# Performance work log

Measured on AMD Instinct MI355X. Metric: run time of the kernel, lower is better.

Reference implementation:

```python
import jax, jax.numpy as jnp
import numpy as np

C_M, C_Z, H, W_LOCAL, G = 256, 128, 8, 32, 16
D = C_M // H  # 32
NEG = -1e9


def setup_inputs() -> dict:
    key = jax.random.key(0)
    ks = jax.random.split(key, 12)
    B, S, N = 1, 32, 512
    s = 0.02
    return {
        "msa": jax.random.normal(ks[0], (B, S, N, C_M), jnp.float32),
        "pair": jax.random.normal(ks[1], (B, N, N, C_Z), jnp.float32),
        "w_q": jax.random.normal(ks[2], (C_M, C_M), jnp.float32) * s,
        "b_q": jnp.zeros((C_M,), jnp.float32),
        "w_k": jax.random.normal(ks[3], (C_M, C_M), jnp.float32) * s,
        "b_k": jnp.zeros((C_M,), jnp.float32),
        "w_v": jax.random.normal(ks[4], (C_M, C_M), jnp.float32) * s,
        "b_v": jnp.zeros((C_M,), jnp.float32),
        "w_o": jax.random.normal(ks[5], (C_M, C_M), jnp.float32) * s,
        "b_o": jnp.zeros((C_M,), jnp.float32),
        "w_b": jax.random.normal(ks[6], (C_Z, H), jnp.float32) * s,
        "b_b": jnp.zeros((H,), jnp.float32),
        "ln_g": jnp.ones((C_M,), jnp.float32),
        "ln_b": jnp.zeros((C_M,), jnp.float32),
    }


def reference(msa, pair, w_q, b_q, w_k, b_k, w_v, b_v, w_o, b_o, w_b, b_b, ln_g, ln_b):
    B, S, N, _ = msa.shape
    # pair bias: [B, N, N, c_z] -> [B, H, N, N]
    bias = jnp.einsum("bnmc,ch->bhnm", pair, w_b) + b_b[None, :, None, None]
    # structured sparsity: local window + global tokens
    i = jnp.arange(N)
    allowed = (jnp.abs(i[:, None] - i[None, :]) <= W_LOCAL // 2) | (i[:, None] < G) | (i[None, :] < G)
    # projections, vectorized over all MSA rows (replaces the per-row python loop)
    q = (msa @ w_q + b_q).reshape(B, S, N, H, D)
    k = (msa @ w_k + b_k).reshape(B, S, N, H, D)
    v = (msa @ w_v + b_v).reshape(B, S, N, H, D)
    scores = jnp.einsum("bsnhd,bsmhd->bshnm", q, k) / jnp.sqrt(jnp.float32(D))
    scores = scores + bias[:, None]  # broadcast over MSA rows
    scores = jnp.where(allowed, scores, NEG)
    attn = jax.nn.softmax(scores, axis=-1)
    out = jnp.einsum("bshnm,bsmhd->bsnhd", attn, v).reshape(B, S, N, C_M)
    out = out @ w_o + b_o
    # residual + LayerNorm over c_m
    y = msa + out
    mu = jnp.mean(y, axis=-1, keepdims=True)
    var = jnp.mean(jnp.square(y - mu), axis=-1, keepdims=True)
    return (y - mu) * jax.lax.rsqrt(var + 1e-5) * ln_g + ln_b
```

## Files before the change

### kernel.cpp

```cpp
#include <hip/hip_runtime.h>
#include <hip/hip_bf16.h>
#include <math.h>

#define NH      8
#define HD      32
#define NN      512
#define SS      32
#define CM      256
#define CZ      128
#define NG      16
#define W_HALF  16
#define MROWS   (SS * NN)

typedef __attribute__((ext_vector_type(8))) __bf16 bf16x8;
typedef __attribute__((ext_vector_type(4))) float f32x4;

__device__ inline unsigned short f2bf(float x) {
    __hip_bfloat16 h = __float2bfloat16(x);
    return __builtin_bit_cast(unsigned short, h);
}
__device__ inline float bflo(unsigned u) { return __uint_as_float(u << 16); }
__device__ inline float bfhi(unsigned u) { return __uint_as_float(u & 0xffff0000u); }
__device__ inline float bf1(unsigned short u) { return __uint_as_float((unsigned)u << 16); }

__global__ __launch_bounds__(256) void cvt_msa_kernel(
    const float* __restrict__ in, unsigned short* __restrict__ out)
{
    int i = (blockIdx.x * 256 + threadIdx.x) * 8;
    const float4* p = reinterpret_cast<const float4*>(in + i);
    float4 v0 = p[0], v1 = p[1];
    union { unsigned short u[8]; uint4 q; } o;
    o.u[0] = f2bf(v0.x); o.u[1] = f2bf(v0.y); o.u[2] = f2bf(v0.z); o.u[3] = f2bf(v0.w);
    o.u[4] = f2bf(v1.x); o.u[5] = f2bf(v1.y); o.u[6] = f2bf(v1.z); o.u[7] = f2bf(v1.w);
    *reinterpret_cast<uint4*>(out + i) = o.q;
}

__global__ __launch_bounds__(256) void cvt_wT_kernel(
    const float* __restrict__ w0, const float* __restrict__ w1,
    const float* __restrict__ w2, const float* __restrict__ w3,
    unsigned short* __restrict__ o0, unsigned short* __restrict__ o1,
    unsigned short* __restrict__ o2, unsigned short* __restrict__ o3)
{
    int mat = blockIdx.y;
    const float* in = (mat == 0) ? w0 : (mat == 1) ? w1 : (mat == 2) ? w2 : w3;
    unsigned short* out = (mat == 0) ? o0 : (mat == 1) ? o1 : (mat == 2) ? o2 : o3;
    int o = blockIdx.x * 256 + threadIdx.x;
    int n = o >> 8, k = o & 255;
    out[o] = f2bf(in[k * 256 + n]);
}

#define JOBS_D  (512 * 33)
#define JOBS_G  (512 * 16)
#define JOBS_R  (512 * 16)
#define NJOBS   (JOBS_D + JOBS_G + JOBS_R)

__global__ __launch_bounds__(256) void bias_kernel(
    const float* __restrict__ pair,
    const float* __restrict__ w_b,
    const float* __restrict__ b_b,
    float* __restrict__ biasD,
    float* __restrict__ biasG,
    float* __restrict__ biasR)
{
    const int t = threadIdx.x;
    const int wave = t >> 6, lane = t & 63;
    int job = blockIdx.x * 4 + wave;
    if (job >= NJOBS) return;

    int n, m;
    float* oaddr;
    int hstride;
    if (job < JOBS_D) {
        n = job / 33;
        int o = job - n * 33;
        m = n + o - 16;
        if (m < 0 || m >= 512) return;
        oaddr = biasD + o * 512 + n;
        hstride = 33 * 512;
    } else if (job < JOBS_D + JOBS_G) {
        int i = job - JOBS_D;
        n = i >> 4; m = i & 15;
        oaddr = biasG + m * 512 + n;
        hstride = 16 * 512;
    } else {
        int i = job - (JOBS_D + JOBS_G);
        n = i & 15; m = i >> 4;
        oaddr = biasR + n * 512 + m;
        hstride = 16 * 512;
    }

    const float2 pv = *reinterpret_cast<const float2*>(
        pair + ((size_t)n * 512 + m) * CZ + 2 * lane);
    const float4 a0 = ((const float4*)(w_b + (2 * lane) * NH))[0];
    const float4 a1 = ((const float4*)(w_b + (2 * lane) * NH))[1];
    const float4 b0 = ((const float4*)(w_b + (2 * lane + 1) * NH))[0];
    const float4 b1 = ((const float4*)(w_b + (2 * lane + 1) * NH))[1];

    float acc8[8];
    acc8[0] = pv.x * a0.x + pv.y * b0.x;
    acc8[1] = pv.x * a0.y + pv.y * b0.y;
    acc8[2] = pv.x * a0.z + pv.y * b0.z;
    acc8[3] = pv.x * a0.w + pv.y * b0.w;
    acc8[4] = pv.x * a1.x + pv.y * b1.x;
    acc8[5] = pv.x * a1.y + pv.y * b1.y;
    acc8[6] = pv.x * a1.z + pv.y * b1.z;
    acc8[7] = pv.x * a1.w + pv.y * b1.w;
#pragma unroll
    for (int h = 0; h < 8; ++h) {
#pragma unroll
        for (int off = 1; off < 64; off <<= 1)
            acc8[h] += __shfl_xor(acc8[h], off, 64);
    }
    if (lane < 8) {
        float v = acc8[0];
#pragma unroll
        for (int h = 1; h < 8; ++h) v = (lane == h) ? acc8[h] : v;
        oaddr[(size_t)lane * hstride] = v + b_b[lane];
    }
}

template <bool RESID, bool BF16OUT>
__global__ __launch_bounds__(256) void mfma_gemm_kernel(
    const unsigned short* __restrict__ A,
    const unsigned short* __restrict__ WT,
    const float* __restrict__ bias,
    const float* __restrict__ resid,
    void* __restrict__ Cout)
{
    __shared__ __align__(16) unsigned short lds[12288];

    const int t = threadIdx.x;
    const int l = t & 63;
    const int w = t >> 6;
    const int wm = w >> 1, wn = w & 1;
    const int bn0 = blockIdx.x * 64;
    const int bm0 = blockIdx.y * 128;

    f32x4 acc[4][2] = {};

    for (int k0 = 0; k0 < 256; k0 += 64) {
#pragma unroll
        for (int j = 0; j < 4; ++j) {
            int Lbase = (j * 4 + w) * 1024;
            int L = Lbase + l * 16;
            int row = L >> 7;
            int cs = (L >> 4) & 7;
            int c = cs ^ (row & 7);
            const unsigned short* gp = A + (size_t)(bm0 + row) * 256 + k0 + c * 8;
            __builtin_amdgcn_global_load_lds(
                (const __attribute__((address_space(1))) void*)gp,
                (__attribute__((address_space(3))) void*)((char*)lds + Lbase), 16, 0, 0);
        }
#pragma unroll
        for (int j = 0; j < 2; ++j) {
            int Lbase = 16384 + (j * 4 + w) * 1024;
            int L = (Lbase - 16384) + l * 16;
            int row = L >> 7;
            int cs = (L >> 4) & 7;
            int c = cs ^ (row & 7);
            const unsigned short* gp = WT + (size_t)(bn0 + row) * 256 + k0 + c * 8;
            __builtin_amdgcn_global_load_lds(
                (const __attribute__((address_space(1))) void*)gp,
                (__attribute__((address_space(3))) void*)((char*)lds + Lbase), 16, 0, 0);
        }
        __syncthreads();

#pragma unroll
        for (int kh = 0; kh < 2; ++kh) {
            bf16x8 a[4], b[2];
#pragma unroll
            for (int m = 0; m < 4; ++m) {
                int row = wm * 64 + m * 16 + (l & 15);
                int c = (kh * 4 + (l >> 4)) ^ (row & 7);
                a[m] = *reinterpret_cast<const bf16x8*>((const char*)lds + row * 128 + c * 16);
            }
#pragma unroll
            for (int nf = 0; nf < 2; ++nf) {
                int nr = wn * 32 + nf * 16 + (l & 15);
                int c = (kh * 4 + (l >> 4)) ^ (nr & 7);
                b[nf] = *reinterpret_cast<const bf16x8*>((const char*)lds + 16384 + nr * 128 + c * 16);
            }
#pragma unroll
            for (int m = 0; m < 4; ++m)
#pragma unroll
                for (int nf = 0; nf < 2; ++nf)
                    acc[m][nf] = __builtin_amdgcn_mfma_f32_16x16x32_bf16(a[m], b[nf], acc[m][nf], 0, 0, 0);
        }
        __syncthreads();
    }

#pragma unroll
    for (int m = 0; m < 4; ++m) {
#pragma unroll
        for (int nf = 0; nf < 2; ++nf) {
            int col = bn0 + wn * 32 + nf * 16 + (l & 15);
            float bv = bias[col];
#pragma unroll
            for (int r = 0; r < 4; ++r) {
                int row = bm0 + wm * 64 + m * 16 + (l >> 4) * 4 + r;
                float val = acc[m][nf][r] + bv;
                if (RESID) val += resid[(size_t)row * 256 + col];
                if (BF16OUT)
                    ((unsigned short*)Cout)[(size_t)row * 256 + col] = f2bf(val);
                else
                    ((float*)Cout)[(size_t)row * 256 + col] = val;
            }
        }
    }
}

__global__ __launch_bounds__(512) void attn2_kernel(
    const unsigned short* __restrict__ qb,
    const unsigned short* __restrict__ kb,
    const unsigned short* __restrict__ vb,
    const float* __restrict__ biasD,
    const float* __restrict__ biasG,
    const float* __restrict__ biasR,
    unsigned short* __restrict__ outp)
{
    __shared__ unsigned short kT[32][512];
    __shared__ unsigned short vT[32][512];

    const int t = threadIdx.x;
    const int h = blockIdx.x >> 5;
    const int s = blockIdx.x & 31;
    const float scale = 0.17677669529663687f;

    {
        const unsigned short* kr = kb + ((size_t)((s << 9) + t)) * 256 + h * 32;
        const unsigned short* vr = vb + ((size_t)((s << 9) + t)) * 256 + h * 32;
        union { uint4 q4[4]; unsigned short u[32]; } kk, vv;
#pragma unroll
        for (int i = 0; i < 4; ++i) {
            kk.q4[i] = ((const uint4*)kr)[i];
            vv.q4[i] = ((const uint4*)vr)[i];
        }
#pragma unroll
        for (int d = 0; d < 32; ++d) {
            kT[d][t] = kk.u[d];
            vT[d][t] = vv.u[d];
        }
    }
    __syncthreads();

    if (blockIdx.y == 0) {
        const int q = t;
        if (q < 16) return;

        float qr[32];
        {
            const unsigned short* qrow = qb + ((size_t)((s << 9) + q)) * 256 + h * 32;
            union { uint4 q4[4]; unsigned short u[32]; } qq;
#pragma unroll
            for (int i = 0; i < 4; ++i) qq.q4[i] = ((const uint4*)qrow)[i];
#pragma unroll
            for (int d = 0; d < 32; ++d) qr[d] = bf1(qq.u[d]) * scale;
        }

        float m_run = -1e30f, l_run = 0.f;
        float acc[32];
#pragma unroll
        for (int d = 0; d < 32; ++d) acc[d] = 0.f;

        const float* bG = biasG + (size_t)(h * 16) * 512 + q;
        for (int i = 0; i < 8; ++i) {
            const int m0 = 2 * i;
            float s0 = 0.f, s1 = 0.f;
#pragma unroll
            for (int d = 0; d < 32; ++d) {
                unsigned u = *(const unsigned*)&kT[d][m0];
                s0 = fmaf(qr[d], bflo(u), s0);
                s1 = fmaf(qr[d], bfhi(u), s1);
            }
            float x0 = s0 + bG[(size_t)m0 * 512];
            float x1 = s1 + bG[(size_t)(m0 + 1) * 512];
            float mx = fmaxf(x0, x1);
            if (mx > m_run) {
                float corr = __expf(m_run - mx);
                m_run = mx; l_run *= corr;
#pragma unroll
                for (int d = 0; d < 32; ++d) acc[d] *= corr;
            }
            float e0 = __expf(x0 - m_run);
            float e1 = __expf(x1 - m_run);
            l_run += e0 + e1;
#pragma unroll
            for (int d = 0; d < 32; ++d) {
                unsigned u = *(const unsigned*)&vT[d][m0];
                acc[d] = fmaf(e0, bflo(u), acc[d]);
                acc[d] = fmaf(e1, bfhi(u), acc[d]);
            }
        }

        const int lo = (q - 16 < 16) ? 16 : q - 16;
        const int hi = (q + 16 > 511) ? 511 : q + 16;
        const int start = (q - 16) & ~1;
        const float* bD = biasD + (size_t)(h * 33) * 512 + q;
        for (int i = 0; i < 18; ++i) {
            const int m0 = start + 2 * i;
            const int mc = (m0 > 510) ? 510 : m0;
            const bool v0 = (m0 >= lo) & (m0 <= hi);
            const bool v1 = (m0 + 1 >= lo) & (m0 + 1 <= hi);
            float s0 = 0.f, s1 = 0.f;
#pragma unroll
            for (int d = 0; d < 32; ++d) {
                unsigned u = *(const unsigned*)&kT[d][mc];
                s0 = fmaf(qr[d], bflo(u), s0);
                s1 = fmaf(qr[d], bfhi(u), s1);
            }
            int o0 = m0 - q + 16;     o0 = o0 < 0 ? 0 : (o0 > 32 ? 32 : o0);
            int o1 = m0 + 1 - q + 16; o1 = o1 < 0 ? 0 : (o1 > 32 ? 32 : o1);
            float x0 = v0 ? (s0 + bD[(size_t)o0 * 512]) : -1e30f;
            float x1 = v1 ? (s1 + bD[(size_t)o1 * 512]) : -1e30f;
            float mx = fmaxf(x0, x1);
            if (mx > m_run) {
                float corr = __expf(m_run - mx);
                m_run = mx; l_run *= corr;
#pragma unroll
                for (int d = 0; d < 32; ++d) acc[d] *= corr;
            }
            float e0 = v0 ? __expf(x0 - m_run) : 0.f;
            float e1 = v1 ? __expf(x1 - m_run) : 0.f;
            l_run += e0 + e1;
#pragma unroll
            for (int d = 0; d < 32; ++d) {
                unsigned u = *(const unsigned*)&vT[d][mc];
                acc[d] = fmaf(e0, bflo(u), acc[d]);
                acc[d] = fmaf(e1, bfhi(u), acc[d]);
            }
        }

        const float inv = 1.0f / l_run;
        union { uint4 q4[4]; unsigned short u[32]; } oo;
#pragma unroll
        for (int d = 0; d < 32; ++d) oo.u[d] = f2bf(acc[d] * inv);
        unsigned short* orow = outp + ((size_t)((s << 9) + q)) * 256 + h * 32;
#pragma unroll
        for (int i = 0; i < 4; ++i) ((uint4*)orow)[i] = oo.q4[i];
    } else {
        const int wv = t >> 6, lane = t & 63;
        for (int qi = 0; qi < 2; ++qi) {
            const int q = wv * 2 + qi;
            float qr[32];
            {
                const unsigned short* qrow = qb + ((size_t)((s << 9) + q)) * 256 + h * 32;
                union { uint4 q4[4]; unsigned short u[32]; } qq;
#pragma unroll
                for (int i = 0; i < 4; ++i) qq.q4[i] = ((const uint4*)qrow)[i];
#pragma unroll
                for (int d = 0; d < 32; ++d) qr[d] = bf1(qq.u[d]) * scale;
            }
            float m_loc = -1e30f, l_loc = 0.f;
            float accl[32];
#pragma unroll
            for (int d = 0; d < 32; ++d) accl[d] = 0.f;

            const float* bR = biasR + (size_t)(h * 16 + q) * 512;
            for (int j = 0; j < 8; ++j) {
                const int m = j * 64 + lane;
                float sc = 0.f;
#pragma unroll
                for (int d = 0; d < 32; ++d)
                    sc = fmaf(qr[d], bf1(kT[d][m]), sc);
                float x = sc + bR[m];
                if (x > m_loc) {
                    float corr = __expf(m_loc - x);
                    m_loc = x; l_loc *= corr;
#pragma unroll
                    for (int d = 0; d < 32; ++d) accl[d] *= corr;
                }
                float e = __expf(x - m_loc);
                l_loc += e;
#pragma unroll
                for (int d = 0; d < 32; ++d)
                    accl[d] = fmaf(e, bf1(vT[d][m]), accl[d]);
            }
            float mg = m_loc;
#pragma unroll
            for (int off = 1; off < 64; off <<= 1)
                mg = fmaxf(mg, __shfl_xor(mg, off, 64));
            float cf = __expf(m_loc - mg);
            float lg = l_loc * cf;
#pragma unroll
            for (int off = 1; off < 64; off <<= 1)
                lg += __shfl_xor(lg, off, 64);
            const float inv = 1.0f / lg;
            union { uint4 q4[4]; unsigned short u[32]; } oo;
#pragma unroll
            for (int d = 0; d < 32; ++d) {
                float a = accl[d] * cf;
#pragma unroll
                for (int off = 1; off < 64; off <<= 1)
                    a += __shfl_xor(a, off, 64);
                oo.u[d] = f2bf(a * inv);
            }
            if (lane == 0) {
                unsigned short* orow = outp + ((size_t)((s << 9) + q)) * 256 + h * 32;
#pragma unroll
                for (int i = 0; i < 4; ++i) ((uint4*)orow)[i] = oo.q4[i];
            }
        }
    }
}

__global__ __launch_bounds__(256) void ln_kernel(
    const float* __restrict__ y,
    const float* __restrict__ g,
    const float* __restrict__ b,
    float* __restrict__ outp)
{
    int t = threadIdx.x;
    int wave = t >> 6, lane = t & 63;
    int row = blockIdx.x * 4 + wave;

    const float4 yv = *reinterpret_cast<const float4*>(y + (size_t)row * CM + lane * 4);
    float s  = yv.x + yv.y + yv.z + yv.w;
    float sq = yv.x * yv.x + yv.y * yv.y + yv.z * yv.z + yv.w * yv.w;
#pragma unroll
    for (int off = 1; off < 64; off <<= 1) {
        s  += __shfl_xor(s, off, 64);
        sq += __shfl_xor(sq, off, 64);
    }
    float mu  = s * (1.0f / CM);
    float var = sq * (1.0f / CM) - mu * mu;
    float r   = rsqrtf(var + 1e-5f);

    float4 gv = *reinterpret_cast<const float4*>(g + lane * 4);
    float4 bv = *reinterpret_cast<const float4*>(b + lane * 4);
    float4 o;
    o.x = (yv.x - mu) * r * gv.x + bv.x;
    o.y = (yv.y - mu) * r * gv.y + bv.y;
    o.z = (yv.z - mu) * r * gv.z + bv.z;
    o.w = (yv.w - mu) * r * gv.w + bv.w;
    *reinterpret_cast<float4*>(outp + (size_t)row * CM + lane * 4) = o;
}

extern "C" void kernel_launch(void* const* d_in, const int* in_sizes, int n_in,
                              void* d_out, int out_size, void* d_ws, size_t ws_size,
                              hipStream_t stream)
{
    const float* msa  = (const float*)d_in[0];
    const float* pair = (const float*)d_in[1];
    const float* w_q  = (const float*)d_in[2];
    const float* b_q  = (const float*)d_in[3];
    const float* w_k  = (const float*)d_in[4];
    const float* b_k  = (const float*)d_in[5];
    const float* w_v  = (const float*)d_in[6];
    const float* b_v  = (const float*)d_in[7];
    const float* w_o  = (const float*)d_in[8];
    const float* b_o  = (const float*)d_in[9];
    const float* w_b  = (const float*)d_in[10];
    const float* b_b  = (const float*)d_in[11];
    const float* ln_g = (const float*)d_in[12];
    const float* ln_b = (const float*)d_in[13];
    float* out = (float*)d_out;

    float* ws    = (float*)d_ws;
    float* biasD = ws;
    float* biasG = biasD + 8 * 33 * 512;
    float* biasR = biasG + 8 * 16 * 512;
    unsigned short* q_bf   = (unsigned short*)(biasR + 8 * 16 * 512);
    unsigned short* k_bf   = q_bf + (size_t)MROWS * CM;
    unsigned short* v_bf   = k_bf + (size_t)MROWS * CM;
    unsigned short* msa_bf = v_bf + (size_t)MROWS * CM;
    unsigned short* ao_bf  = msa_bf + (size_t)MROWS * CM;
    unsigned short* wqT = ao_bf + (size_t)MROWS * CM;
    unsigned short* wkT = wqT + CM * CM;
    unsigned short* wvT = wkT + CM * CM;
    unsigned short* woT = wvT + CM * CM;

    cvt_msa_kernel<<<(MROWS * CM) / (256 * 8), 256, 0, stream>>>(msa, msa_bf);
    cvt_wT_kernel<<<dim3(CM * CM / 256, 4), 256, 0, stream>>>(
        w_q, w_k, w_v, w_o, wqT, wkT, wvT, woT);

    bias_kernel<<<(NJOBS + 3) / 4, 256, 0, stream>>>(
        pair, w_b, b_b, biasD, biasG, biasR);

    dim3 gg(CM / 64, MROWS / 128);
    mfma_gemm_kernel<false, true><<<gg, 256, 0, stream>>>(msa_bf, wqT, b_q, nullptr, q_bf);
    mfma_gemm_kernel<false, true><<<gg, 256, 0, stream>>>(msa_bf, wkT, b_k, nullptr, k_bf);
    mfma_gemm_kernel<false, true><<<gg, 256, 0, stream>>>(msa_bf, wvT, b_v, nullptr, v_bf);

    attn2_kernel<<<dim3(256, 2), 512, 0, stream>>>(
        q_bf, k_bf, v_bf, biasD, biasG, biasR, ao_bf);

    mfma_gemm_kernel<true, false><<<gg, 256, 0, stream>>>(ao_bf, woT, b_o, msa, out);

    ln_kernel<<<MROWS / 4, 256, 0, stream>>>(out, ln_g, ln_b, out);
}
```

Baseline: 311.4 us.

## Fuse Q/K/V projections into one GEMM and double-buffer LDS staging

Replaces the three separate Q, K and V projection launches with a single kernel. Each block loads the shared msa tile once and multiplies it against all three transposed weight tiles, so A-operand traffic and launch count drop. Both this kernel and the output-projection GEMM now use a two-buffer LDS schedule with the K loop fully unrolled, issuing the next k-slice's async global-to-LDS loads while MFMAs run on the current one. In exchange, per-block LDS grows to 80 KB for QKV, which limits blocks per CU. The QKV kernel also holds three times as many accumulators, which raises register pressure.

```diff
diff --git a/kernel.cpp b/kernel.cpp
--- a/kernel.cpp
+++ b/kernel.cpp
@@ -119,15 +119,63 @@
     }
 }
 
-template <bool RESID, bool BF16OUT>
-__global__ __launch_bounds__(256) void mfma_gemm_kernel(
+#define STAGE_A(bufbase, k0)                                                 \
+    _Pragma("unroll")                                                        \
+    for (int j = 0; j < 4; ++j) {                                            \
+        int Lrel = (j * 4 + w) * 1024;                                       \
+        int L = Lrel + l * 16;                                               \
+        int row = L >> 7;                                                    \
+        int c = ((L >> 4) & 7) ^ (row & 7);                                  \
+        const unsigned short* gp = A + (size_t)(bm0 + row) * 256 + (k0) + c * 8; \
+        __builtin_amdgcn_global_load_lds(                                    \
+            (const __attribute__((address_space(1))) void*)gp,               \
+            (__attribute__((address_space(3))) void*)((char*)lds + (bufbase) + Lrel), 16, 0, 0); \
+    }
+
+#define STAGE_B(bufbase, Bofs, WTP, k0)                                      \
+    _Pragma("unroll")                                                        \
+    for (int j = 0; j < 2; ++j) {                                            \
+        int Lrel = (j * 4 + w) * 1024;                                       \
+        int L = Lrel + l * 16;                                               \
+        int row = L >> 7;                                                    \
+        int c = ((L >> 4) & 7) ^ (row & 7);                                  \
+        const unsigned short* gp = (WTP) + (size_t)(bn0 + row) * 256 + (k0) + c * 8; \
+        __builtin_amdgcn_global_load_lds(                                    \
+            (const __attribute__((address_space(1))) void*)gp,               \
+            (__attribute__((address_space(3))) void*)((char*)lds + (bufbase) + (Bofs) + Lrel), 16, 0, 0); \
+    }
+
+#define LOAD_AFRAG(afr, bufbase, kh)                                         \
+    _Pragma("unroll")                                                        \
+    for (int m = 0; m < 4; ++m) {                                            \
+        int row = wm * 64 + m * 16 + (l & 15);                               \
+        int c = ((kh) * 4 + (l >> 4)) ^ (row & 7);                           \
+        afr[m] = *reinterpret_cast<const bf16x8*>(                           \
+            (const char*)lds + (bufbase) + row * 128 + c * 16);              \
+    }
+
+#define LOAD_BFRAG(bfr, bufbase, Bofs, kh)                                   \
+    _Pragma("unroll")                                                        \
+    for (int nf = 0; nf < 2; ++nf) {                                         \
+        int nr = wn * 32 + nf * 16 + (l & 15);                               \
+        int c = ((kh) * 4 + (l >> 4)) ^ (nr & 7);                            \
+        bfr[nf] = *reinterpret_cast<const bf16x8*>(                          \
+            (const char*)lds + (bufbase) + (Bofs) + nr * 128 + c * 16);      \
+    }
+
+__global__ __launch_bounds__(256) void qkv_gemm_kernel(
     const unsigned short* __restrict__ A,
-    const unsigned short* __restrict__ WT,
-    const float* __restrict__ bias,
-    const float* __restrict__ resid,
-    void* __restrict__ Cout)
-{
-    __shared__ __align__(16) unsigned short lds[12288];
+    const unsigned short* __restrict__ WT0,
+    const unsigned short* __restrict__ WT1,
+    const unsigned short* __restrict__ WT2,
+    const float* __restrict__ bq,
+    const float* __restrict__ bk,
+    const float* __restrict__ bv,
+    unsigned short* __restrict__ Oq,
+    unsigned short* __restrict__ Ok,
+    unsigned short* __restrict__ Ov)
+{
+    __shared__ __align__(16) unsigned short lds[40960];
 
     const int t = threadIdx.x;
     const int l = t & 63;
@@ -136,58 +184,121 @@
     const int bn0 = blockIdx.x * 64;
     const int bm0 = blockIdx.y * 128;
 
+    const unsigned short* WT[3] = {WT0, WT1, WT2};
+    f32x4 acc[3][4][2] = {};
+
+#define QKV_STAGE(bufbase, k0)                                               \
+    {                                                                        \
+        STAGE_A(bufbase, k0)                                                 \
+        _Pragma("unroll")                                                    \
+        for (int widx = 0; widx < 3; ++widx) {                               \
+            STAGE_B(bufbase, 16384 + widx * 8192, WT[widx], k0)              \
+        }                                                                    \
+    }
+
+#define QKV_COMPUTE(bufbase)                                                 \
+    _Pragma("unroll")                                                        \
+    for (int kh = 0; kh < 2; ++kh) {                                         \
+        bf16x8 a[4];                                                         \
+        LOAD_AFRAG(a, bufbase, kh)                                           \
+        _Pragma("unroll")                                                    \
+        for (int widx = 0; widx < 3; ++widx) {                               \
+            bf16x8 b[2];                                                     \
+            LOAD_BFRAG(b, bufbase, 16384 + widx * 8192, kh)                  \
+            _Pragma("unroll")                                                \
+            for (int m = 0; m < 4; ++m)                                      \
+                _Pragma("unroll")                                            \
+                for (int nf = 0; nf < 2; ++nf)                               \
+                    acc[widx][m][nf] = __builtin_amdgcn_mfma_f32_16x16x32_bf16( \
+                        a[m], b[nf], acc[widx][m][nf], 0, 0, 0);             \
+        }                                                                    \
+    }
+
+    QKV_STAGE(0, 0)
+    __syncthreads();
+    QKV_STAGE(40960, 64)
+    QKV_COMPUTE(0)
+    __syncthreads();
+    QKV_STAGE(0, 128)
+    QKV_COMPUTE(40960)
+    __syncthreads();
+    QKV_STAGE(40960, 192)
+    QKV_COMPUTE(0)
+    __syncthreads();
+    QKV_COMPUTE(40960)
+
+    const float* bptr[3] = {bq, bk, bv};
+    unsigned short* optr[3] = {Oq, Ok, Ov};
+#pragma unroll
+    for (int widx = 0; widx < 3; ++widx) {
+#pragma unroll
+        for (int m = 0; m < 4; ++m) {
+#pragma unroll
+            for (int nf = 0; nf < 2; ++nf) {
+                int col = bn0 + wn * 32 + nf * 16 + (l & 15);
+                float bv_ = bptr[widx][col];
+#pragma unroll
+                for (int r = 0; r < 4; ++r) {
+                    int row = bm0 + wm * 64 + m * 16 + (l >> 4) * 4 + r;
+                    optr[widx][(size_t)row * 256 + col] = f2bf(acc[widx][m][nf][r] + bv_);
+                }
+            }
+        }
+    }
+#undef QKV_STAGE
+#undef QKV_COMPUTE
+}
+
+__global__ __launch_bounds__(256) void out_gemm_kernel(
+    const unsigned short* __restrict__ A,
+    const unsigned short* __restrict__ WTp,
+    const float* __restrict__ bias,
+    const float* __restrict__ resid,
+    float* __restrict__ C)
+{
+    __shared__ __align__(16) unsigned short lds[24576];
+
+    const int t = threadIdx.x;
+    const int l = t & 63;
+    const int w = t >> 6;
+    const int wm = w >> 1, wn = w & 1;
+    const int bn0 = blockIdx.x * 64;
+    const int bm0 = blockIdx.y * 128;
+
     f32x4 acc[4][2] = {};
 
-    for (int k0 = 0; k0 < 256; k0 += 64) {
-#pragma unroll
-        for (int j = 0; j < 4; ++j) {
-            int Lbase = (j * 4 + w) * 1024;
-            int L = Lbase + l * 16;
-            int row = L >> 7;
-            int cs = (L >> 4) & 7;
-            int c = cs ^ (row & 7);
-            const unsigned short* gp = A + (size_t)(bm0 + row) * 256 + k0 + c * 8;
-            __builtin_amdgcn_global_load_lds(
-                (const __attribute__((address_space(1))) void*)gp,
-                (__attribute__((address_space(3))) void*)((char*)lds + Lbase), 16, 0, 0);
-        }
-#pragma unroll
-        for (int j = 0; j < 2; ++j) {
-            int Lbase = 16384 + (j * 4 + w) * 1024;
-            int L = (Lbase - 16384) + l * 16;
-            int row = L >> 7;
-            int cs = (L >> 4) & 7;
-            int c = cs ^ (row & 7);
-            const unsigned short* gp = WT + (size_t)(bn0 + row) * 256 + k0 + c * 8;
-            __builtin_amdgcn_global_load_lds(
-                (const __attribute__((address_space(1))) void*)gp,
-                (__attribute__((address_space(3))) void*)((char*)lds + Lbase), 16, 0, 0);
-        }
-        __syncthreads();
-
-#pragma unroll
-        for (int kh = 0; kh < 2; ++kh) {
-            bf16x8 a[4], b[2];
-#pragma unroll
-            for (int m = 0; m < 4; ++m) {
-                int row = wm * 64 + m * 16 + (l & 15);
-                int c = (kh * 4 + (l >> 4)) ^ (row & 7);
-                a[m] = *reinterpret_cast<const bf16x8*>((const char*)lds + row * 128 + c * 16);
-            }
-#pragma unroll
-            for (int nf = 0; nf < 2; ++nf) {
-                int nr = wn * 32 + nf * 16 + (l & 15);
-                int c = (kh * 4 + (l >> 4)) ^ (nr & 7);
-                b[nf] = *reinterpret_cast<const bf16x8*>((const char*)lds + 16384 + nr * 128 + c * 16);
-            }
-#pragma unroll
-            for (int m = 0; m < 4; ++m)
-#pragma unroll
-                for (int nf = 0; nf < 2; ++nf)
-                    acc[m][nf] = __builtin_amdgcn_mfma_f32_16x16x32_bf16(a[m], b[nf], acc[m][nf], 0, 0, 0);
-        }
-        __syncthreads();
-    }
+#define OUT_STAGE(bufbase, k0)                                               \
+    {                                                                        \
+        STAGE_A(bufbase, k0)                                                 \
+        STAGE_B(bufbase, 16384, WTp, k0)                                     \
+    }
+
+#define OUT_COMPUTE(bufbase)                                                 \
+    _Pragma("unroll")                                                        \
+    for (int kh = 0; kh < 2; ++kh) {                                         \
+        bf16x8 a[4], b[2];                                                   \
+        LOAD_AFRAG(a, bufbase, kh)                                           \
+        LOAD_BFRAG(b, bufbase, 16384, kh)                                    \
+        _Pragma("unroll")                                                    \
+        for (int m = 0; m < 4; ++m)                                          \
+            _Pragma("unroll")                                                \
+            for (int nf = 0; nf < 2; ++nf)                                   \
+                acc[m][nf] = __builtin_amdgcn_mfma_f32_16x16x32_bf16(        \
+                    a[m], b[nf], acc[m][nf], 0, 0, 0);                       \
+    }
+
+    OUT_STAGE(0, 0)
+    __syncthreads();
+    OUT_STAGE(24576, 64)
+    OUT_COMPUTE(0)
+    __syncthreads();
+    OUT_STAGE(0, 128)
+    OUT_COMPUTE(24576)
+    __syncthreads();
+    OUT_STAGE(24576, 192)
+    OUT_COMPUTE(0)
+    __syncthreads();
+    OUT_COMPUTE(24576)
 
 #pragma unroll
     for (int m = 0; m < 4; ++m) {
@@ -198,15 +309,13 @@
 #pragma unroll
             for (int r = 0; r < 4; ++r) {
                 int row = bm0 + wm * 64 + m * 16 + (l >> 4) * 4 + r;
-                float val = acc[m][nf][r] + bv;
-                if (RESID) val += resid[(size_t)row * 256 + col];
-                if (BF16OUT)
-                    ((unsigned short*)Cout)[(size_t)row * 256 + col] = f2bf(val);
-                else
-                    ((float*)Cout)[(size_t)row * 256 + col] = val;
-            }
-        }
-    }
+                C[(size_t)row * 256 + col] =
+                    acc[m][nf][r] + bv + resid[(size_t)row * 256 + col];
+            }
+        }
+    }
+#undef OUT_STAGE
+#undef OUT_COMPUTE
 }
 
 __global__ __launch_bounds__(512) void attn2_kernel(
@@ -477,14 +586,13 @@
         pair, w_b, b_b, biasD, biasG, biasR);
 
     dim3 gg(CM / 64, MROWS / 128);
-    mfma_gemm_kernel<false, true><<<gg, 256, 0, stream>>>(msa_bf, wqT, b_q, nullptr, q_bf);
-    mfma_gemm_kernel<false, true><<<gg, 256, 0, stream>>>(msa_bf, wkT, b_k, nullptr, k_bf);
-    mfma_gemm_kernel<false, true><<<gg, 256, 0, stream>>>(msa_bf, wvT, b_v, nullptr, v_bf);
+    qkv_gemm_kernel<<<gg, 256, 0, stream>>>(
+        msa_bf, wqT, wkT, wvT, b_q, b_k, b_v, q_bf, k_bf, v_bf);
 
     attn2_kernel<<<dim3(256, 2), 512, 0, stream>>>(
         q_bf, k_bf, v_bf, biasD, biasG, biasR, ao_bf);
 
-    mfma_gemm_kernel<true, false><<<gg, 256, 0, stream>>>(ao_bf, woT, b_o, msa, out);
+    out_gemm_kernel<<<gg, 256, 0, stream>>>(ao_bf, woT, b_o, msa, out);
 
     ln_kernel<<<MROWS / 4, 256, 0, stream>>>(out, ln_g, ln_b, out);
 }
```

After: 306.7 us. About the same (-1.5%).
